# Performance work log

Measured on AMD Instinct MI355X. Metric: run time of the kernel, lower is better.

## Reference

```python
import jax, jax.numpy as jnp
import numpy as np

N_E = 16384
E_DIM = 64
GROUPS = 4
N_E_GROUP = N_E // GROUPS  # 4096
B, H, W = 16, 32, 32


def _l2norm(x):
    # matches F.normalize(p=2, dim=-1) with eps=1e-12
    n = jnp.linalg.norm(x, axis=-1, keepdims=True)
    return x / jnp.maximum(n, 1e-12)


def setup_inputs() -> dict:
    key = jax.random.key(0)
    k1, k2 = jax.random.split(key)
    z_groups = jax.random.normal(k1, (B, GROUPS * E_DIM, H, W), dtype=jnp.float32)
    emb = jax.random.uniform(k2, (N_E, E_DIM), minval=-1.0 / N_E, maxval=1.0 / N_E,
                             dtype=jnp.float32)
    emb = _l2norm(emb)  # module normalizes codebook at init when l2_norm=True
    return {"z_groups": z_groups, "embedding": emb}


def reference(z_groups, embedding):
    # Eval-mode forward (no EMA/random-restart buffer updates, losses are 0).
    b, c, h, w = z_groups.shape
    # split channels into groups: b (g*c) h w -> b h w g c
    z = z_groups.reshape(b, GROUPS, E_DIM, h, w).transpose(0, 3, 4, 1, 2)
    z = _l2norm(z)                                     # l2_norm=True path
    zf = z.reshape(-1, GROUPS, E_DIM)                  # [N, g, c]
    emb = _l2norm(embedding.reshape(GROUPS, N_E_GROUP, E_DIM))  # [g, k, c]

    # d = -|z|^2 - |e|^2 + 2 z.e  (negative squared distance), argmax = nearest
    d = (2.0 * jnp.einsum('ngc,gkc->ngk', zf, emb)
         - jnp.sum(zf * zf, axis=-1)[..., None]
         - jnp.sum(emb * emb, axis=-1)[None, :, :])    # [N, g, k]
    idx = jnp.argmax(d, axis=-1)                       # [N, g]

    zq = emb[jnp.arange(GROUPS)[None, :], idx]         # [N, g, c] gather
    zq = zf + jax.lax.stop_gradient(zq - zf)           # straight-through

    # b h w g c -> b (g*c) h w
    quant = zq.reshape(b, h, w, GROUPS, E_DIM).transpose(0, 3, 4, 1, 2)
    quant = quant.reshape(b, GROUPS * E_DIM, h, w)

    vq_loss = jnp.zeros((GROUPS,), jnp.float32)
    commit_loss = jnp.zeros((GROUPS,), jnp.float32)
    codebook_usage = jnp.zeros((GROUPS,), jnp.float32)

    # perplexity / min_encodings correspond to the last group (loop semantics)
    min_encodings = jax.nn.one_hot(idx[:, -1], N_E_GROUP, dtype=quant.dtype)
    avg_probs = jnp.mean(min_encodings, axis=0)
    perplexity = jnp.exp(-jnp.sum(avg_probs * jnp.log(avg_probs + 1e-10)))

    return (quant, vq_loss, commit_loss, codebook_usage,
            perplexity, min_encodings, idx)
```

## Files before the change

### kernel.cpp

```cpp
#include <hip/hip_runtime.h>
#include <hip/hip_bf16.h>
#include <math.h>

#define N_E      16384
#define E_DIM    64
#define GROUPS   4
#define N_E_G    4096
#define NQ       16384

#define OFF_QUANT   0L
#define OFF_VQLOSS  4194304L
#define OFF_PERP    4194316L
#define OFF_MINENC  4194317L
#define OFF_IDX     71303181L

#define WS_EN     0L
#define WS_EN2    1048576L
#define WS_ENHI   1064960L
#define WS_ZNR    1589248L
#define WS_ZHI    5783552L
#define WS_HIST   7880704L
#define WS_IDX3   7884800L

typedef float  float4v  __attribute__((ext_vector_type(4)));
typedef short  short8   __attribute__((ext_vector_type(8)));

static __device__ __forceinline__ ushort f2bf(float x) {
    union { __hip_bfloat16 h; ushort u; } cv; cv.h = __float2bfloat16(x);
    return cv.u;
}

__global__ void norm_all_kernel(const float* __restrict__ emb,
                                const float* __restrict__ z,
                                float* __restrict__ en, float* __restrict__ en2,
                                ushort* __restrict__ ehi,
                                float* __restrict__ znr, ushort* __restrict__ zhi) {
    __shared__ float tile[64 * 65];
    __shared__ float rden[64];
    const int t = threadIdx.x;

    if (blockIdx.x < 4096) {
        int gid  = blockIdx.x * 256 + t;
        int code = gid >> 6;
        int lane = t & 63;
        float x = emb[code * 64 + lane];
        float ss = x * x;
        #pragma unroll
        for (int off = 32; off; off >>= 1) ss += __shfl_xor(ss, off, 64);
        float v = x / fmaxf(sqrtf(ss), 1e-12f);
        en[code * 64 + lane]  = v;
        ehi[code * 64 + lane] = f2bf(v);
        float s2 = v * v;
        #pragma unroll
        for (int off = 32; off; off >>= 1) s2 += __shfl_xor(s2, off, 64);
        if (lane == 0) en2[code] = s2;
        return;
    }

    int bx2 = blockIdx.x - 4096;
    int g   = bx2 >> 8;
    int n0  = (bx2 & 255) * 64;
    int b   = n0 >> 10, hw0 = n0 & 1023;
    const float* src = z + (size_t)b * 262144 + (size_t)g * 65536 + hw0;

    for (int i = t; i < 4096; i += 256) {
        int d = i >> 6, nl = i & 63;
        tile[d * 65 + nl] = src[(size_t)d * 1024 + nl];
    }
    __syncthreads();

    if (t < 64) {
        float ss = 0.f;
        for (int d = 0; d < 64; ++d) {
            float x = tile[d * 65 + t];
            ss = fmaf(x, x, ss);
        }
        rden[t] = fmaxf(sqrtf(ss), 1e-12f);
    }
    __syncthreads();

    for (int i = t; i < 4096; i += 256) {
        int q = i >> 6, d = i & 63;
        float v = tile[d * 65 + q] / rden[q];
        size_t o = ((size_t)g * NQ + n0 + q) * 64 + d;
        znr[o] = v;
        zhi[o] = f2bf(v);
    }
}

#define CAP  64
#define TAU  0.017f
__global__ __launch_bounds__(256, 2)
void vq_cand_kernel(const ushort* __restrict__ zhi, const ushort* __restrict__ ehi,
                    const float* __restrict__ znr, const float* __restrict__ en,
                    const float* __restrict__ en2, float* __restrict__ out,
                    int* __restrict__ hist, int* __restrict__ idx3) {
    __shared__ int    cnt[128];
    __shared__ ushort cand[128 * CAP];
    __shared__ int    bks[128];

    const int g  = blockIdx.y;
    const int q0 = blockIdx.x * 128;
    const int t  = threadIdx.x;
    const int wave = t >> 6, lane = t & 63;
    const int l15 = lane & 15, quad = lane >> 4;
    const int qhalf = wave & 1, chalf = wave >> 1;

    const int sliceId = blockIdx.y * (NQ / 128) + blockIdx.x;
    float4v* fill4 = (float4v*)(out + OFF_VQLOSS) + (size_t)sliceId * 32768;

    if (t < 128) cnt[t] = 0;

    short8 bfrag[4][2];
    {
        const ushort* zq = zhi + ((size_t)g * NQ + q0 + qhalf * 64 + l15) * 64 + quad * 8;
        #pragma unroll
        for (int u = 0; u < 4; ++u)
            #pragma unroll
            for (int ks = 0; ks < 2; ++ks)
                bfrag[u][ks] = *(const short8*)(zq + u * 16 * 64 + ks * 32);
    }
    __syncthreads();

    const ushort* abase = ehi + (size_t)g * N_E_G * 64
                        + (size_t)(chalf * 64 + l15) * 64 + quad * 8;

    float Mrun[4];
    #pragma unroll
    for (int u = 0; u < 4; ++u) Mrun[u] = -3.4e38f;

    short8 afA[4][2], afB[4][2];
    #pragma unroll
    for (int cs = 0; cs < 4; ++cs)
        #pragma unroll
        for (int ks = 0; ks < 2; ++ks)
            afA[cs][ks] = *(const short8*)(abase + (size_t)(cs * 16) * 64 + ks * 32);

    auto do_tile = [&](short8 (&A)[4][2], short8 (&P)[4][2], int tile) {
        if (tile + 1 < 32) {
            const ushort* p = abase + (size_t)((tile + 1) * 128) * 64;
            #pragma unroll
            for (int cs = 0; cs < 4; ++cs)
                #pragma unroll
                for (int ks = 0; ks < 2; ++ks)
                    P[cs][ks] = *(const short8*)(p + (size_t)(cs * 16) * 64 + ks * 32);
        }
        {
            const float4v z4 = {0.f, 0.f, 0.f, 0.f};
            #pragma unroll
            for (int r = 0; r < 4; ++r)
                fill4[(size_t)(tile * 4 + r) * 256 + t] = z4;
        }
        float4v acc[4][4];
        #pragma unroll
        for (int cs = 0; cs < 4; ++cs)
            #pragma unroll
            for (int u = 0; u < 4; ++u) {
                float4v zz = {0.f, 0.f, 0.f, 0.f};
                float4v tmp = __builtin_amdgcn_mfma_f32_16x16x32_bf16(
                                  A[cs][0], bfrag[u][0], zz, 0, 0, 0);
                acc[cs][u] = __builtin_amdgcn_mfma_f32_16x16x32_bf16(
                                  A[cs][1], bfrag[u][1], tmp, 0, 0, 0);
            }
        const int j0 = tile * 128;
        #pragma unroll
        for (int u = 0; u < 4; ++u) {
            float m = acc[0][u][0];
            #pragma unroll
            for (int cs = 0; cs < 4; ++cs)
                #pragma unroll
                for (int r = 0; r < 4; ++r) m = fmaxf(m, acc[cs][u][r]);
            float m2 = fmaxf(m, __shfl_xor(m, 16, 64));
            float m4 = fmaxf(m2, __shfl_xor(m2, 32, 64));
            Mrun[u] = fmaxf(Mrun[u], m4);
            float thr = Mrun[u] - TAU;
            if (m >= thr) {
                int ql = qhalf * 64 + u * 16 + l15;
                #pragma unroll
                for (int cs = 0; cs < 4; ++cs)
                    #pragma unroll
                    for (int r = 0; r < 4; ++r)
                        if (acc[cs][u][r] >= thr) {
                            int cidx = j0 + chalf * 64 + cs * 16 + quad * 4 + r;
                            int slot = atomicAdd(&cnt[ql], 1);
                            if (slot < CAP) cand[ql * CAP + slot] = (ushort)cidx;
                        }
            }
        }
    };

    for (int tt = 0; tt < 32; tt += 2) {
        do_tile(afA, afB, tt);
        do_tile(afB, afA, tt + 1);
    }

    if (sliceId == 0 && t < 13) out[OFF_VQLOSS + 67108864L + t] = 0.f;
    __syncthreads();

    if (t < 128) {
        int q = q0 + t;
        float za[64];
        const float4v* zp = (const float4v*)(znr + ((size_t)g * NQ + q) * 64);
        #pragma unroll
        for (int i = 0; i < 16; ++i) {
            float4v v = zp[i];
            za[i*4+0] = v[0]; za[i*4+1] = v[1]; za[i*4+2] = v[2]; za[i*4+3] = v[3];
        }
        int nc = cnt[t]; if (nc > CAP) nc = CAP;
        float best = -3.4e38f; int bk = 0x7fffffff;
        for (int s = 0; s < nc; ++s) {
            int c = cand[t * CAP + s];
            const float* ev = en + ((size_t)g * N_E_G + c) * 64;
            float a = 0.f;
            #pragma unroll
            for (int k = 0; k < 64; ++k) a = fmaf(za[k], ev[k], a);
            float d = 2.f * a - en2[g * N_E_G + c];
            if (d > best || (d == best && c < bk)) { best = d; bk = c; }
        }
        if (bk == 0x7fffffff) bk = 0;
        bks[t] = bk;
        out[OFF_IDX + (size_t)q * 4 + g] = (float)bk;
        if (g == 3) {
            idx3[q] = bk;
            atomicAdd(&hist[bk], 1);
        }
    }
    __syncthreads();

    for (int i = t; i < 128 * 64; i += 256) {
        int d = i >> 7, m = i & 127;
        int n = q0 + m, b = n >> 10, hw = n & 1023;
        out[OFF_QUANT + (size_t)b * 262144 + (size_t)(g * 64 + d) * 1024 + hw] =
            en[((size_t)g * N_E_G + bks[m]) * 64 + d];
    }
}

__global__ void finalize_kernel(const int* __restrict__ idx3,
                                const int* __restrict__ hist,
                                float* __restrict__ out) {
    if (blockIdx.x < 64) {
        int r = blockIdx.x * 256 + threadIdx.x;
        out[OFF_MINENC + (size_t)r * N_E_G + idx3[r]] = 1.0f;
        return;
    }
    __shared__ float s[256];
    int t = threadIdx.x;
    float acc = 0.f;
    for (int k = t; k < N_E_G; k += 256) {
        float p = (float)hist[k] * (1.0f / 16384.0f);
        acc += p * logf(p + 1e-10f);
    }
    s[t] = acc;
    __syncthreads();
    for (int o = 128; o; o >>= 1) {
        if (t < o) s[t] += s[t + o];
        __syncthreads();
    }
    if (t == 0) out[OFF_PERP] = expf(-s[0]);
}

extern "C" void kernel_launch(void* const* d_in, const int* in_sizes, int n_in,
                              void* d_out, int out_size, void* d_ws, size_t ws_size,
                              hipStream_t stream) {
    const float* z_groups = (const float*)d_in[0];
    const float* emb      = (const float*)d_in[1];
    float* out = (float*)d_out;
    float* ws  = (float*)d_ws;

    float*  en   = ws + WS_EN;
    float*  en2  = ws + WS_EN2;
    ushort* ehi  = (ushort*)(ws + WS_ENHI);
    float*  znr  = ws + WS_ZNR;
    ushort* zhi  = (ushort*)(ws + WS_ZHI);
    int*    hist = (int*)(ws + WS_HIST);
    int*    idx3 = (int*)(ws + WS_IDX3);

    hipMemsetAsync(hist, 0, N_E_G * sizeof(int), stream);

    norm_all_kernel<<<4096 + 1024, 256, 0, stream>>>(emb, z_groups,
                                                     en, en2, ehi, znr, zhi);

    vq_cand_kernel<<<dim3(NQ / 128, GROUPS), 256, 0, stream>>>(
        zhi, ehi, znr, en, en2, out, hist, idx3);

    finalize_kernel<<<65, 256, 0, stream>>>(idx3, hist, out);
}
```

Before: 402.0 us.

## Fuse z normalization into candidate kernel via shared-memory transpose

Moves the per-query z L2 normalization and transpose out of the preprocessing kernel and into the VQ candidate kernel, where each block loads its 128 queries, normalizes them in LDS and builds bf16 MFMA fragments from LDS. This removes the round-trip writes and reads of the fp32 and bf16 normalized z workspaces (about 24 MB). Shared memory grows to roughly 35 KB per block through a union, which may affect the two-blocks-per-CU occupancy target. The per-tile max reduction is also restructured into a tree of fmaxf.

```diff
diff --git a/kernel.cpp b/kernel.cpp
--- a/kernel.cpp
+++ b/kernel.cpp
@@ -17,8 +17,6 @@
 #define WS_EN     0L
 #define WS_EN2    1048576L
 #define WS_ENHI   1064960L
-#define WS_ZNR    1589248L
-#define WS_ZHI    5783552L
 #define WS_HIST   7880704L
 #define WS_IDX3   7884800L
 
@@ -30,74 +28,46 @@
     return cv.u;
 }
 
-__global__ void norm_all_kernel(const float* __restrict__ emb,
-                                const float* __restrict__ z,
+__global__ void norm_emb_kernel(const float* __restrict__ emb,
                                 float* __restrict__ en, float* __restrict__ en2,
-                                ushort* __restrict__ ehi,
-                                float* __restrict__ znr, ushort* __restrict__ zhi) {
-    __shared__ float tile[64 * 65];
-    __shared__ float rden[64];
+                                ushort* __restrict__ ehi) {
     const int t = threadIdx.x;
-
-    if (blockIdx.x < 4096) {
-        int gid  = blockIdx.x * 256 + t;
-        int code = gid >> 6;
-        int lane = t & 63;
-        float x = emb[code * 64 + lane];
-        float ss = x * x;
-        #pragma unroll
-        for (int off = 32; off; off >>= 1) ss += __shfl_xor(ss, off, 64);
-        float v = x / fmaxf(sqrtf(ss), 1e-12f);
-        en[code * 64 + lane]  = v;
-        ehi[code * 64 + lane] = f2bf(v);
-        float s2 = v * v;
-        #pragma unroll
-        for (int off = 32; off; off >>= 1) s2 += __shfl_xor(s2, off, 64);
-        if (lane == 0) en2[code] = s2;
-        return;
-    }
-
-    int bx2 = blockIdx.x - 4096;
-    int g   = bx2 >> 8;
-    int n0  = (bx2 & 255) * 64;
-    int b   = n0 >> 10, hw0 = n0 & 1023;
-    const float* src = z + (size_t)b * 262144 + (size_t)g * 65536 + hw0;
-
-    for (int i = t; i < 4096; i += 256) {
-        int d = i >> 6, nl = i & 63;
-        tile[d * 65 + nl] = src[(size_t)d * 1024 + nl];
-    }
-    __syncthreads();
-
-    if (t < 64) {
-        float ss = 0.f;
-        for (int d = 0; d < 64; ++d) {
-            float x = tile[d * 65 + t];
-            ss = fmaf(x, x, ss);
-        }
-        rden[t] = fmaxf(sqrtf(ss), 1e-12f);
-    }
-    __syncthreads();
-
-    for (int i = t; i < 4096; i += 256) {
-        int q = i >> 6, d = i & 63;
-        float v = tile[d * 65 + q] / rden[q];
-        size_t o = ((size_t)g * NQ + n0 + q) * 64 + d;
-        znr[o] = v;
-        zhi[o] = f2bf(v);
-    }
+    int gid  = blockIdx.x * 256 + t;
+    int code = gid >> 6;
+    int lane = t & 63;
+    float x = emb[code * 64 + lane];
+    float ss = x * x;
+    #pragma unroll
+    for (int off = 32; off; off >>= 1) ss += __shfl_xor(ss, off, 64);
+    float v = x / fmaxf(sqrtf(ss), 1e-12f);
+    en[code * 64 + lane]  = v;
+    ehi[code * 64 + lane] = f2bf(v);
+    float s2 = v * v;
+    #pragma unroll
+    for (int off = 32; off; off >>= 1) s2 += __shfl_xor(s2, off, 64);
+    if (lane == 0) en2[code] = s2;
 }
 
 #define CAP  64
 #define TAU  0.017f
+#define ZSTR 68
+
 __global__ __launch_bounds__(256, 2)
-void vq_cand_kernel(const ushort* __restrict__ zhi, const ushort* __restrict__ ehi,
-                    const float* __restrict__ znr, const float* __restrict__ en,
+void vq_cand_kernel(const float* __restrict__ z,
+                    const ushort* __restrict__ ehi,
+                    const float* __restrict__ en,
                     const float* __restrict__ en2, float* __restrict__ out,
                     int* __restrict__ hist, int* __restrict__ idx3) {
-    __shared__ int    cnt[128];
-    __shared__ ushort cand[128 * CAP];
-    __shared__ int    bks[128];
+    __shared__ float zn[128 * ZSTR];
+    __shared__ float rden[128];
+    __shared__ union {
+        float tile[64 * 129];
+        struct {
+            ushort cand[128 * CAP];
+            int    cnt[128];
+            int    bks[128];
+        } kl;
+    } sh;
 
     const int g  = blockIdx.y;
     const int q0 = blockIdx.x * 128;
@@ -109,32 +79,63 @@
     const int sliceId = blockIdx.y * (NQ / 128) + blockIdx.x;
     float4v* fill4 = (float4v*)(out + OFF_VQLOSS) + (size_t)sliceId * 32768;
 
-    if (t < 128) cnt[t] = 0;
-
-    short8 bfrag[4][2];
-    {
-        const ushort* zq = zhi + ((size_t)g * NQ + q0 + qhalf * 64 + l15) * 64 + quad * 8;
-        #pragma unroll
-        for (int u = 0; u < 4; ++u)
-            #pragma unroll
-            for (int ks = 0; ks < 2; ++ks)
-                bfrag[u][ks] = *(const short8*)(zq + u * 16 * 64 + ks * 32);
-    }
-    __syncthreads();
-
     const ushort* abase = ehi + (size_t)g * N_E_G * 64
                         + (size_t)(chalf * 64 + l15) * 64 + quad * 8;
-
-    float Mrun[4];
-    #pragma unroll
-    for (int u = 0; u < 4; ++u) Mrun[u] = -3.4e38f;
-
     short8 afA[4][2], afB[4][2];
     #pragma unroll
     for (int cs = 0; cs < 4; ++cs)
         #pragma unroll
         for (int ks = 0; ks < 2; ++ks)
             afA[cs][ks] = *(const short8*)(abase + (size_t)(cs * 16) * 64 + ks * 32);
+
+    {
+        const int b = q0 >> 10, hw0 = q0 & 1023;
+        const float* src = z + (size_t)b * 262144 + (size_t)g * 65536 + hw0;
+        for (int i = t; i < 8192; i += 256) {
+            int d = i >> 7, nq = i & 127;
+            sh.tile[d * 129 + nq] = src[(size_t)d * 1024 + nq];
+        }
+        __syncthreads();
+        if (t < 128) {
+            float ss = 0.f;
+            for (int d = 0; d < 64; ++d) {
+                float x = sh.tile[d * 129 + t];
+                ss = fmaf(x, x, ss);
+            }
+            rden[t] = fmaxf(sqrtf(ss), 1e-12f);
+        }
+        __syncthreads();
+        for (int i = t; i < 8192; i += 256) {
+            int q = i >> 6, d = i & 63;
+            zn[q * ZSTR + d] = sh.tile[d * 129 + q] / rden[q];
+        }
+        __syncthreads();
+    }
+
+    if (t < 128) sh.kl.cnt[t] = 0;
+
+    short8 bfrag[4][2];
+    #pragma unroll
+    for (int uu = 0; uu < 4; ++uu) {
+        int ql = qhalf * 64 + uu * 16 + l15;
+        #pragma unroll
+        for (int ks = 0; ks < 2; ++ks) {
+            const float* p = &zn[ql * ZSTR + ks * 32 + quad * 8];
+            float4v a = *(const float4v*)p;
+            float4v c = *(const float4v*)(p + 4);
+            short8 f;
+            f[0] = (short)f2bf(a[0]); f[1] = (short)f2bf(a[1]);
+            f[2] = (short)f2bf(a[2]); f[3] = (short)f2bf(a[3]);
+            f[4] = (short)f2bf(c[0]); f[5] = (short)f2bf(c[1]);
+            f[6] = (short)f2bf(c[2]); f[7] = (short)f2bf(c[3]);
+            bfrag[uu][ks] = f;
+        }
+    }
+    __syncthreads();
+
+    float Mrun[4];
+    #pragma unroll
+    for (int u = 0; u < 4; ++u) Mrun[u] = -3.4e38f;
 
     auto do_tile = [&](short8 (&A)[4][2], short8 (&P)[4][2], int tile) {
         if (tile + 1 < 32) {
@@ -165,14 +166,18 @@
         const int j0 = tile * 128;
         #pragma unroll
         for (int u = 0; u < 4; ++u) {
-            float m = acc[0][u][0];
-            #pragma unroll
-            for (int cs = 0; cs < 4; ++cs)
-                #pragma unroll
-                for (int r = 0; r < 4; ++r) m = fmaxf(m, acc[cs][u][r]);
-            float m2 = fmaxf(m, __shfl_xor(m, 16, 64));
-            float m4 = fmaxf(m2, __shfl_xor(m2, 32, 64));
-            Mrun[u] = fmaxf(Mrun[u], m4);
+            float m0 = fmaxf(fmaxf(acc[0][u][0], acc[0][u][1]),
+                             fmaxf(acc[0][u][2], acc[0][u][3]));
+            float m1 = fmaxf(fmaxf(acc[1][u][0], acc[1][u][1]),
+                             fmaxf(acc[1][u][2], acc[1][u][3]));
+            float m2 = fmaxf(fmaxf(acc[2][u][0], acc[2][u][1]),
+                             fmaxf(acc[2][u][2], acc[2][u][3]));
+            float m3 = fmaxf(fmaxf(acc[3][u][0], acc[3][u][1]),
+                             fmaxf(acc[3][u][2], acc[3][u][3]));
+            float m  = fmaxf(fmaxf(m0, m1), fmaxf(m2, m3));
+            float mh = fmaxf(m,  __shfl_xor(m,  16, 64));
+            float mw = fmaxf(mh, __shfl_xor(mh, 32, 64));
+            Mrun[u] = fmaxf(Mrun[u], mw);
             float thr = Mrun[u] - TAU;
             if (m >= thr) {
                 int ql = qhalf * 64 + u * 16 + l15;
@@ -182,8 +187,8 @@
                     for (int r = 0; r < 4; ++r)
                         if (acc[cs][u][r] >= thr) {
                             int cidx = j0 + chalf * 64 + cs * 16 + quad * 4 + r;
-                            int slot = atomicAdd(&cnt[ql], 1);
-                            if (slot < CAP) cand[ql * CAP + slot] = (ushort)cidx;
+                            int slot = atomicAdd(&sh.kl.cnt[ql], 1);
+                            if (slot < CAP) sh.kl.cand[ql * CAP + slot] = (ushort)cidx;
                         }
             }
         }
@@ -200,16 +205,16 @@
     if (t < 128) {
         int q = q0 + t;
         float za[64];
-        const float4v* zp = (const float4v*)(znr + ((size_t)g * NQ + q) * 64);
+        const float4v* zp = (const float4v*)(&zn[t * ZSTR]);
         #pragma unroll
         for (int i = 0; i < 16; ++i) {
             float4v v = zp[i];
             za[i*4+0] = v[0]; za[i*4+1] = v[1]; za[i*4+2] = v[2]; za[i*4+3] = v[3];
         }
-        int nc = cnt[t]; if (nc > CAP) nc = CAP;
+        int nc = sh.kl.cnt[t]; if (nc > CAP) nc = CAP;
         float best = -3.4e38f; int bk = 0x7fffffff;
         for (int s = 0; s < nc; ++s) {
-            int c = cand[t * CAP + s];
+            int c = sh.kl.cand[t * CAP + s];
             const float* ev = en + ((size_t)g * N_E_G + c) * 64;
             float a = 0.f;
             #pragma unroll
@@ -218,7 +223,7 @@
             if (d > best || (d == best && c < bk)) { best = d; bk = c; }
         }
         if (bk == 0x7fffffff) bk = 0;
-        bks[t] = bk;
+        sh.kl.bks[t] = bk;
         out[OFF_IDX + (size_t)q * 4 + g] = (float)bk;
         if (g == 3) {
             idx3[q] = bk;
@@ -231,7 +236,7 @@
         int d = i >> 7, m = i & 127;
         int n = q0 + m, b = n >> 10, hw = n & 1023;
         out[OFF_QUANT + (size_t)b * 262144 + (size_t)(g * 64 + d) * 1024 + hw] =
-            en[((size_t)g * N_E_G + bks[m]) * 64 + d];
+            en[((size_t)g * N_E_G + sh.kl.bks[m]) * 64 + d];
     }
 }
 
@@ -270,18 +275,15 @@
     float*  en   = ws + WS_EN;
     float*  en2  = ws + WS_EN2;
     ushort* ehi  = (ushort*)(ws + WS_ENHI);
-    float*  znr  = ws + WS_ZNR;
-    ushort* zhi  = (ushort*)(ws + WS_ZHI);
     int*    hist = (int*)(ws + WS_HIST);
     int*    idx3 = (int*)(ws + WS_IDX3);
 
     hipMemsetAsync(hist, 0, N_E_G * sizeof(int), stream);
 
-    norm_all_kernel<<<4096 + 1024, 256, 0, stream>>>(emb, z_groups,
-                                                     en, en2, ehi, znr, zhi);
+    norm_emb_kernel<<<4096, 256, 0, stream>>>(emb, en, en2, ehi);
 
     vq_cand_kernel<<<dim3(NQ / 128, GROUPS), 256, 0, stream>>>(
-        zhi, ehi, znr, en, en2, out, hist, idx3);
+        z_groups, ehi, en, en2, out, hist, idx3);
 
     finalize_kernel<<<65, 256, 0, stream>>>(idx3, hist, out);
 }
```

New measurement: 394.6 us. Within noise of the previous version (-1.9%).
